# Kernel tuning notes

Measured on AMD Instinct MI355X. Metric: run time of the kernel, lower is better.

Reference implementation:

```python
import jax, jax.numpy as jnp
import numpy as np

N, M, D = 2048, 2048, 128


def setup_inputs() -> dict:
    key = jax.random.key(0)
    kx, ky = jax.random.split(key)
    x = jax.random.normal(kx, (N, D), dtype=jnp.float32)
    y = jax.random.normal(ky, (M, D), dtype=jnp.float32)
    return {"x": x, "y": y}


def reference(x, y):
    # negative pairwise L1 distance: -sum_d |x[n,d] - y[m,d]| -> [N, M]
    return -jnp.sum(jnp.abs(x[:, None, :] - y[None, :, :]), axis=-1)
```

## Files before the change

### kernel.cpp

```cpp
#include <hip/hip_runtime.h>


typedef float f4 __attribute__((ext_vector_type(4)));
typedef __attribute__((address_space(4))) const f4 cf4;

#define DD 128
#define ROWS 16
#define NCH 4

__launch_bounds__(256)
__global__ void l1_dist_kernel(const float* __restrict__ X,
                               const float* __restrict__ Y,
                               float* __restrict__ out,
                               int N, int M) {
    const int wave = __builtin_amdgcn_readfirstlane((int)(threadIdx.x >> 6));
    const int lane = threadIdx.x & 63;
    const int gw = blockIdx.x * 4 + wave;
    const int mg = gw & 31;
    const int rg = gw >> 5;
    const int m  = mg * 64 + lane;
    const int n0 = rg * ROWS;

    float acc[ROWS];
#pragma unroll
    for (int r = 0; r < ROWS; ++r) acc[r] = 0.f;

#pragma unroll
    for (int c = 0; c < NCH; ++c) {
        f4 yv[8];
        const f4* yp = (const f4*)(Y + (size_t)m * DD + c * 32);
#pragma unroll
        for (int k = 0; k < 8; ++k) yv[k] = yp[k];

#pragma unroll
        for (int r = 0; r < ROWS; ++r) {
            cf4* xp = (cf4*)(X + (size_t)(n0 + r) * DD + c * 32);
            float a0 = 0.f, a1 = 0.f, a2 = 0.f, a3 = 0.f;
#pragma unroll
            for (int k = 0; k < 8; ++k) {
                f4 xv = xp[k];
                a0 += __builtin_fabsf(xv.x - yv[k].x);
                a1 += __builtin_fabsf(xv.y - yv[k].y);
                a2 += __builtin_fabsf(xv.z - yv[k].z);
                a3 += __builtin_fabsf(xv.w - yv[k].w);
            }
            acc[r] += (a0 + a1) + (a2 + a3);
        }
    }

#pragma unroll
    for (int r = 0; r < ROWS; ++r)
        out[(size_t)(n0 + r) * M + m] = -acc[r];
}

extern "C" void kernel_launch(void* const* d_in, const int* in_sizes, int n_in,
                              void* d_out, int out_size, void* d_ws, size_t ws_size,
                              hipStream_t stream) {
    const float* x = (const float*)d_in[0];
    const float* y = (const float*)d_in[1];
    float* out = (float*)d_out;
    const int N = in_sizes[0] / DD;
    const int M = in_sizes[1] / DD;
    const int waves = (M / 64) * (N / ROWS);
    dim3 grid(waves / 4);
    l1_dist_kernel<<<grid, 256, 0, stream>>>(x, y, out, N, M);
}
```

Before: 32.55 us.

## Stage X rows in shared memory and tile blocks in 2D

X rows were previously read through scalar (constant address space) loads, which are wave-uniform. Now each block cooperatively loads a 32x128 tile of X into LDS and reads it from there. The grid becomes 2D (128 columns by 32 rows), so each block's four waves share the X tile across two column halves. The change also adds launch-bound occupancy hints and stops unrolling the chunk loop. The risk is that the former scalar loads were nearly free, while LDS broadcast reads now compete with the VALU work and add a barrier.

```diff
diff --git a/kernel.cpp b/kernel.cpp
--- a/kernel.cpp
+++ b/kernel.cpp
@@ -2,30 +2,41 @@
 
 
 typedef float f4 __attribute__((ext_vector_type(4)));
-typedef __attribute__((address_space(4))) const f4 cf4;
 
 #define DD 128
+#define BR 32
 #define ROWS 16
 #define NCH 4
 
-__launch_bounds__(256)
+__launch_bounds__(256, 4)
 __global__ void l1_dist_kernel(const float* __restrict__ X,
                                const float* __restrict__ Y,
                                float* __restrict__ out,
                                int N, int M) {
-    const int wave = __builtin_amdgcn_readfirstlane((int)(threadIdx.x >> 6));
-    const int lane = threadIdx.x & 63;
-    const int gw = blockIdx.x * 4 + wave;
-    const int mg = gw & 31;
-    const int rg = gw >> 5;
-    const int m  = mg * 64 + lane;
-    const int n0 = rg * ROWS;
+    __shared__ float xs[BR * DD];
+
+    const int tid = threadIdx.x;
+    const int wave = tid >> 6;
+    const int lane = tid & 63;
+    const int brow = blockIdx.y * BR;
+    const int bcol = blockIdx.x * 128;
+    const int wrow = (wave >> 1) * ROWS;
+    const int m = bcol + (wave & 1) * 64 + lane;
+
+#pragma unroll
+    for (int k = 0; k < 4; ++k) {
+        int idx = tid + k * 256;
+        int r = idx >> 5, q = idx & 31;
+        *(f4*)&xs[r * DD + (q << 2)] =
+            *(const f4*)&X[(size_t)(brow + r) * DD + (q << 2)];
+    }
+    __syncthreads();
 
     float acc[ROWS];
 #pragma unroll
     for (int r = 0; r < ROWS; ++r) acc[r] = 0.f;
 
-#pragma unroll
+#pragma unroll 1
     for (int c = 0; c < NCH; ++c) {
         f4 yv[8];
         const f4* yp = (const f4*)(Y + (size_t)m * DD + c * 32);
@@ -34,7 +45,7 @@
 
 #pragma unroll
         for (int r = 0; r < ROWS; ++r) {
-            cf4* xp = (cf4*)(X + (size_t)(n0 + r) * DD + c * 32);
+            const f4* xp = (const f4*)&xs[(wrow + r) * DD + c * 32];
             float a0 = 0.f, a1 = 0.f, a2 = 0.f, a3 = 0.f;
 #pragma unroll
             for (int k = 0; k < 8; ++k) {
@@ -50,7 +61,7 @@
 
 #pragma unroll
     for (int r = 0; r < ROWS; ++r)
-        out[(size_t)(n0 + r) * M + m] = -acc[r];
+        out[(size_t)(brow + wrow + r) * M + m] = -acc[r];
 }
 
 extern "C" void kernel_launch(void* const* d_in, const int* in_sizes, int n_in,
@@ -61,7 +72,6 @@
     float* out = (float*)d_out;
     const int N = in_sizes[0] / DD;
     const int M = in_sizes[1] / DD;
-    const int waves = (M / 64) * (N / ROWS);
-    dim3 grid(waves / 4);
+    dim3 grid(M / 128, N / BR);
     l1_dist_kernel<<<grid, 256, 0, stream>>>(x, y, out, N, M);
 }
```

Result: slower. 50.34 us (+54.6%).
